# Kernel optimization log

Hardware: AMD Instinct MI355X
Metric: run time of the kernel (lower is better)

Reference implementation:

```python
import jax, jax.numpy as jnp
import numpy as np

B, N, E = 8, 2000, 32000
LAT, STY, NF = 128, 64, 10
HEADS, HID = 4, 128
OUT = 3 + NF  # 13
EPS = 1e-5
SLOPE = 0.2


def _lin(k, fi, fo):
    return jax.random.normal(k, (fi, fo), dtype=jnp.float32) / np.sqrt(fi)


def setup_inputs() -> dict:
    key = jax.random.key(0)
    ks = jax.random.split(key, 32)
    inp = {
        'z': jax.random.normal(ks[0], (B, LAT), dtype=jnp.float32),
        'template_x': jax.random.normal(ks[1], (N, NF), dtype=jnp.float32),
        'template_edge_index': jax.random.randint(ks[2], (2, E), 0, N, dtype=jnp.int32),
        # style MLP
        'mlp_w1': _lin(ks[3], LAT, 256), 'mlp_b1': jnp.zeros((256,), jnp.float32),
        'mlp_w2': _lin(ks[4], 256, 512), 'mlp_b2': jnp.zeros((512,), jnp.float32),
        'mlp_w3': _lin(ks[5], 512, STY), 'mlp_b3': jnp.zeros((STY,), jnp.float32),
        # GAT1: in = NF + STY = 74 -> heads*HID = 512, concat
        'gat1_w': _lin(ks[6], NF + STY, HEADS * HID),
        'gat1_as': jax.random.normal(ks[7], (HEADS, HID), jnp.float32) * 0.1,
        'gat1_ad': jax.random.normal(ks[8], (HEADS, HID), jnp.float32) * 0.1,
        'gat1_b': jnp.zeros((HEADS * HID,), jnp.float32),
        'ln1_g': jnp.ones((HEADS * HID,), jnp.float32), 'ln1_b': jnp.zeros((HEADS * HID,), jnp.float32),
        # GAT2: 512 -> 512, concat
        'gat2_w': _lin(ks[9], HEADS * HID, HEADS * HID),
        'gat2_as': jax.random.normal(ks[10], (HEADS, HID), jnp.float32) * 0.1,
        'gat2_ad': jax.random.normal(ks[11], (HEADS, HID), jnp.float32) * 0.1,
        'gat2_b': jnp.zeros((HEADS * HID,), jnp.float32),
        'ln2_g': jnp.ones((HEADS * HID,), jnp.float32), 'ln2_b': jnp.zeros((HEADS * HID,), jnp.float32),
        # GAT3: 512 -> 13, 1 head, no concat
        'gat3_w': _lin(ks[12], HEADS * HID, OUT),
        'gat3_as': jax.random.normal(ks[13], (1, OUT), jnp.float32) * 0.1,
        'gat3_ad': jax.random.normal(ks[14], (1, OUT), jnp.float32) * 0.1,
        'gat3_b': jnp.zeros((OUT,), jnp.float32),
    }
    return inp


def gat_conv(x, src, dst, n_nodes, W, a_src, a_dst, bias, heads, out_ch, concat):
    # x: [NT, F_in]; per-head linear transform
    h = (x @ W).reshape(-1, heads, out_ch)              # [NT, H, C]
    als = jnp.sum(h * a_src[None], axis=-1)             # [NT, H]
    ald = jnp.sum(h * a_dst[None], axis=-1)             # [NT, H]
    logits = jax.nn.leaky_relu(als[src] + ald[dst], SLOPE)   # [E, H]
    # segment softmax over destination nodes (self-loops guarantee nonempty segments)
    mx = jax.ops.segment_max(logits, dst, num_segments=n_nodes)
    alpha = jnp.exp(logits - mx[dst])
    den = jax.ops.segment_sum(alpha, dst, num_segments=n_nodes)
    alpha = alpha / den[dst]                             # [E, H]
    msgs = h[src] * alpha[:, :, None]                    # [E, H, C]
    out = jax.ops.segment_sum(msgs, dst, num_segments=n_nodes)  # [NT, H, C]
    if concat:
        return out.reshape(n_nodes, heads * out_ch) + bias
    return out.mean(axis=1) + bias


def layer_norm(x, g, b):
    mu = jnp.mean(x, axis=-1, keepdims=True)
    var = jnp.mean((x - mu) ** 2, axis=-1, keepdims=True)
    return (x - mu) * jax.lax.rsqrt(var + EPS) * g + b


def reference(z, template_x, template_edge_index,
              mlp_w1, mlp_b1, mlp_w2, mlp_b2, mlp_w3, mlp_b3,
              gat1_w, gat1_as, gat1_ad, gat1_b, ln1_g, ln1_b,
              gat2_w, gat2_as, gat2_ad, gat2_b, ln2_g, ln2_b,
              gat3_w, gat3_as, gat3_ad, gat3_b):
    bsz = z.shape[0]
    n = template_x.shape[0]
    nt = bsz * n
    # batch the template graph: replicate nodes, offset edge indices per graph
    x = jnp.tile(template_x, (bsz, 1))                                  # [NT, NF]
    off = (jnp.arange(bsz, dtype=template_edge_index.dtype) * n)
    ei = (template_edge_index[:, None, :] + off[None, :, None]).reshape(2, -1)  # [2, B*E]
    loops = jnp.arange(nt, dtype=ei.dtype)
    src = jnp.concatenate([ei[0], loops])
    dst = jnp.concatenate([ei[1], loops])
    # style MLP
    s = jax.nn.leaky_relu(z @ mlp_w1 + mlp_b1, SLOPE)
    s = jax.nn.leaky_relu(s @ mlp_w2 + mlp_b2, SLOPE)
    s = s @ mlp_w3 + mlp_b3                                             # [B, STY]
    s_exp = jnp.repeat(s, n, axis=0)                                    # [NT, STY]
    H0 = jnp.concatenate([x, s_exp], axis=1)
    H1 = jax.nn.leaky_relu(gat_conv(H0, src, dst, nt, gat1_w, gat1_as, gat1_ad, gat1_b, HEADS, HID, True), SLOPE)
    H1n = layer_norm(H1, ln1_g, ln1_b)
    H2 = jax.nn.leaky_relu(gat_conv(H1n, src, dst, nt, gat2_w, gat2_as, gat2_ad, gat2_b, HEADS, HID, True), SLOPE)
    H2 = H2 + H1n
    H2n = layer_norm(H2, ln2_g, ln2_b)
    H_out = gat_conv(H2n, src, dst, nt, gat3_w, gat3_as, gat3_ad, gat3_b, 1, OUT, False)  # [NT, 13]
    delta_p = H_out[:, :3]
    delta_f = H_out[:, 3:]
    p_gen = x[:, :3] + delta_p
    X_gen = jnp.concatenate([p_gen, x[:, 3:] + delta_f[:, 3:]], axis=1)  # X[:, :3] overwritten by p_gen
    EF = p_gen[ei[1]] - p_gen[ei[0]]                                     # edge displacement vectors [B*E, 3]
    return X_gen, p_gen, EF
```

## Files before the change

kernel.cpp:

```cpp
#include <hip/hip_runtime.h>

constexpr int Bz = 8, Nn = 2000, Ee = 32000, NTOT = 16000;
constexpr int XG_OFF = 0, PG_OFF = 160000, EF_OFF = 208000;
#define SLOPE 0.2f
#define EPSL 1e-5f

typedef __attribute__((ext_vector_type(8))) short short8v;
typedef __attribute__((ext_vector_type(4))) float float4v;

__device__ __forceinline__ float lrelu(float x) { return x > 0.f ? x : SLOPE * x; }

__device__ __forceinline__ unsigned short f2bf(float x) {
  union { float f; unsigned int u; } v; v.f = x;
  unsigned int r = v.u + 0x7fffu + ((v.u >> 16) & 1u);
  return (unsigned short)(r >> 16);
}
__device__ __forceinline__ float bf2f(unsigned int u) {
  return __uint_as_float(u << 16);
}

__device__ __forceinline__ float wave_max(float v) {
  for (int o = 32; o; o >>= 1) v = fmaxf(v, __shfl_xor(v, o));
  return v;
}
__device__ __forceinline__ float wave_sum(float v) {
  for (int o = 32; o; o >>= 1) v += __shfl_xor(v, o);
  return v;
}

__global__ void hist_k(const int* __restrict__ tei, int* __restrict__ counts) {
  int j = blockIdx.x * 256 + threadIdx.x;
  if (j < Ee) atomicAdd(&counts[tei[Ee + j]], 1);
}

__global__ void scan_k(const int* __restrict__ counts, int* __restrict__ offs) {
  __shared__ int part[256];
  int t = threadIdx.x;
  int loc[8];
  int s = 0;
  for (int i = 0; i < 8; i++) {
    int idx = t * 8 + i;
    int c = (idx < Nn) ? counts[idx] : 0;
    loc[i] = s; s += c;
  }
  part[t] = s;
  __syncthreads();
  for (int o = 1; o < 256; o <<= 1) {
    int v = (t >= o) ? part[t - o] : 0;
    __syncthreads();
    part[t] += v;
    __syncthreads();
  }
  int excl = (t == 0) ? 0 : part[t - 1];
  for (int i = 0; i < 8; i++) {
    int idx = t * 8 + i;
    if (idx < Nn) offs[idx] = excl + loc[i];
  }
  if (t == 255) offs[Nn] = part[255];
}

__global__ void place_k(const int* __restrict__ tei, const int* __restrict__ offs,
                        int* __restrict__ cursor, int* __restrict__ colb) {
  int j = blockIdx.x * 256 + threadIdx.x;
  if (j < Ee) {
    int d = tei[Ee + j];
    int slot = offs[d] + atomicAdd(&cursor[d], 1);
    colb[slot] = tei[j];
  }
}

template <int K, int ACT>
__global__ __launch_bounds__(256) void lin_k(const float* __restrict__ x, const float* __restrict__ w,
                                             const float* __restrict__ bias, float* __restrict__ y,
                                             int O) {
  int gw = blockIdx.x * 4 + (threadIdx.x >> 6);
  int lane = threadIdx.x & 63;
  int bb = gw / O, o = gw - bb * O;
  float acc = 0.f;
#pragma unroll
  for (int k = lane; k < K; k += 64) acc += x[bb * K + k] * w[k * O + o];
  acc = wave_sum(acc);
  if (lane == 0) {
    if (bias) acc += bias[o];
    y[gw] = ACT ? lrelu(acc) : acc;
  }
}

__global__ __launch_bounds__(256) void w2bf_k(const float* __restrict__ W, unsigned short* __restrict__ Bt) {
  __shared__ float tile[32][33];
  int tx = threadIdx.x & 31, ty = threadIdx.x >> 5;
  int x0 = blockIdx.x * 32;
  int y0 = blockIdx.y * 32;
  for (int r = ty; r < 32; r += 8) tile[r][tx] = W[(y0 + r) * 512 + x0 + tx];
  __syncthreads();
  for (int r = ty; r < 32; r += 8) Bt[(x0 + r) * 512 + (y0 + tx)] = f2bf(tile[tx][r]);
}

__global__ void w3t_k(const float* __restrict__ W, unsigned short* __restrict__ W3t) {
  for (int idx = threadIdx.x; idx < 8192; idx += 256) {
    int col = idx >> 9, k = idx & 511;
    float v = (col < 13) ? W[k * 13 + col] : 0.f;
    W3t[idx] = f2bf(v);
  }
}

__global__ __launch_bounds__(256) void h1_k(const float* __restrict__ tx, const float* __restrict__ g1w,
                                            const float* __restrict__ pb,
                                            const float* __restrict__ a_s, const float* __restrict__ a_d,
                                            unsigned short* __restrict__ h1, float* __restrict__ als,
                                            float* __restrict__ ald) {
  int blk = blockIdx.x;
  int b = blk & 7, nl = blk >> 3;
  int n = b * Nn + nl;
  int head = threadIdx.x >> 6, lane = threadIdx.x & 63;
  int c = head * 128 + 2 * lane;
  float t0 = 0.f, t1 = 0.f;
#pragma unroll
  for (int k = 0; k < 10; k++) {
    float xv = tx[nl * 10 + k];
    float2 wv = *(const float2*)&g1w[k * 512 + c];
    t0 += xv * wv.x; t1 += xv * wv.y;
  }
  float2 pv = *(const float2*)&pb[b * 512 + c];
  float hx = t0 + pv.x, hy = t1 + pv.y;
  ushort2 st; st.x = f2bf(hx); st.y = f2bf(hy);
  *(ushort2*)&h1[(size_t)n * 512 + c] = st;
  float2 av = *(const float2*)&a_s[c];
  float2 dv = *(const float2*)&a_d[c];
  float pa = wave_sum(hx * av.x + hy * av.y);
  float pd = wave_sum(hx * dv.x + hy * dv.y);
  if (lane == 0) { als[n * 4 + head] = pa; ald[n * 4 + head] = pd; }
}

template <int RESID>
__global__ __launch_bounds__(256) void agg_k(const unsigned short* __restrict__ h,
                                             const float* __restrict__ als, const float* __restrict__ ald,
                                             const float* __restrict__ bias,
                                             const float* __restrict__ g, const float* __restrict__ beta,
                                             const unsigned short* __restrict__ resid,
                                             unsigned short* __restrict__ out,
                                             const int* __restrict__ offs, const int* __restrict__ colb) {
  int blk = blockIdx.x;
  int b = blk & 7, nl = blk >> 3;
  int n = b * Nn + nl;
  int w = threadIdx.x >> 6, lane = threadIdx.x & 63;
  int li = lane & 15, eg = lane >> 4;
  int rs = offs[nl];
  int nit = offs[nl + 1] - rs + 1;
  float aldn = ald[n * 4 + w];

  __shared__ float alpha_s[4][64];
  __shared__ int sgn[64];
  __shared__ float fin[512];

  float accv[8] = {0.f, 0.f, 0.f, 0.f, 0.f, 0.f, 0.f, 0.f};
  float inv;
  const unsigned short* hbase = h + (size_t)w * 128 + li * 8;

  if (nit <= 64) {
    int sg = n;
    float logit = -3e38f;
    if (lane < nit) {
      sg = (lane < nit - 1) ? colb[rs + lane] + b * Nn : n;
      logit = lrelu(als[sg * 4 + w] + aldn);
      if (w == 0) sgn[lane] = sg;
    }
    float m = wave_max(logit);
    float raw = (lane < nit) ? __expf(logit - m) : 0.f;
    inv = 1.f / wave_sum(raw);
    if (lane < nit) alpha_s[w][lane] = raw;
    __syncthreads();
    for (int e = eg; e < nit; e += 4) {
      float a = alpha_s[w][e];
      uint4 hv = *(const uint4*)(hbase + (size_t)sgn[e] * 512);
      accv[0] += a * bf2f(hv.x & 0xffffu); accv[1] += a * bf2f(hv.x >> 16);
      accv[2] += a * bf2f(hv.y & 0xffffu); accv[3] += a * bf2f(hv.y >> 16);
      accv[4] += a * bf2f(hv.z & 0xffffu); accv[5] += a * bf2f(hv.z >> 16);
      accv[6] += a * bf2f(hv.w & 0xffffu); accv[7] += a * bf2f(hv.w >> 16);
    }
    __syncthreads();
  } else {
    float m = -3e38f;
    for (int i = lane; i < nit; i += 64) {
      int sg = (i < nit - 1) ? colb[rs + i] + b * Nn : n;
      m = fmaxf(m, lrelu(als[sg * 4 + w] + aldn));
    }
    m = wave_max(m);
    float den = 0.f;
    for (int base = 0; base < nit; base += 64) {
      int cnt = min(64, nit - base);
      float raw = 0.f;
      if (lane < cnt) {
        int i = base + lane;
        int sg = (i < nit - 1) ? colb[rs + i] + b * Nn : n;
        raw = __expf(lrelu(als[sg * 4 + w] + aldn) - m);
        if (w == 0) sgn[lane] = sg;
        alpha_s[w][lane] = raw;
      }
      den += raw;
      __syncthreads();
      for (int e = eg; e < cnt; e += 4) {
        float a = alpha_s[w][e];
        uint4 hv = *(const uint4*)(hbase + (size_t)sgn[e] * 512);
        accv[0] += a * bf2f(hv.x & 0xffffu); accv[1] += a * bf2f(hv.x >> 16);
        accv[2] += a * bf2f(hv.y & 0xffffu); accv[3] += a * bf2f(hv.y >> 16);
        accv[4] += a * bf2f(hv.z & 0xffffu); accv[5] += a * bf2f(hv.z >> 16);
        accv[6] += a * bf2f(hv.w & 0xffffu); accv[7] += a * bf2f(hv.w >> 16);
      }
      __syncthreads();
    }
    inv = 1.f / wave_sum(den);
  }

#pragma unroll
  for (int j = 0; j < 8; j++) {
    accv[j] += __shfl_xor(accv[j], 16);
    accv[j] += __shfl_xor(accv[j], 32);
  }
  if (eg == 0) {
#pragma unroll
    for (int j = 0; j < 8; j++) fin[w * 128 + li * 8 + j] = accv[j] * inv;
  }
  __syncthreads();

  int c = 2 * threadIdx.x;
  float v0 = lrelu(fin[c] + bias[c]);
  float v1 = lrelu(fin[c + 1] + bias[c + 1]);
  if (RESID) {
    unsigned int rv = *(const unsigned int*)&resid[(size_t)n * 512 + c];
    v0 += bf2f(rv & 0xffffu); v1 += bf2f(rv >> 16);
  }
  __shared__ float red[8];
  __shared__ float bc[2];
  float p1 = wave_sum(v0 + v1);
  float p2 = wave_sum(v0 * v0 + v1 * v1);
  if (lane == 0) { red[w] = p1; red[4 + w] = p2; }
  __syncthreads();
  if (threadIdx.x == 0) {
    float s1 = red[0] + red[1] + red[2] + red[3];
    float s2 = red[4] + red[5] + red[6] + red[7];
    float mu = s1 * (1.f / 512.f);
    float var = s2 * (1.f / 512.f) - mu * mu;
    bc[0] = mu;
    bc[1] = rsqrtf(var + EPSL);
  }
  __syncthreads();
  float mu = bc[0], rstd = bc[1];
  float o0 = (v0 - mu) * rstd * g[c] + beta[c];
  float o1 = (v1 - mu) * rstd * g[c + 1] + beta[c + 1];
  ushort2 st; st.x = f2bf(o0); st.y = f2bf(o1);
  *(ushort2*)&out[(size_t)n * 512 + c] = st;
}

__global__ __launch_bounds__(256) void gemm2_k(const unsigned short* __restrict__ A,
                                               const unsigned short* __restrict__ Bt,
                                               unsigned short* __restrict__ C,
                                               const float* __restrict__ As, const float* __restrict__ Ad,
                                               float* __restrict__ als2, float* __restrict__ ald2) {
  __shared__ char smem[32768];
  char* sAc = smem;
  char* sBc = smem + 16384;
  int t = threadIdx.x;
  int lane = t & 63, w = t >> 6;
  int wr = w >> 1, wc = w & 1;
  int m0 = blockIdx.y * 128, n0 = blockIdx.x * 128;
  int head = blockIdx.x;

  float4v acc[4][4];
#pragma unroll
  for (int i = 0; i < 4; i++)
#pragma unroll
    for (int j = 0; j < 4; j++) acc[i][j] = (float4v){0.f, 0.f, 0.f, 0.f};

  int srow[4], sklin[4], ssw[4];
#pragma unroll
  for (int i = 0; i < 4; i++) {
    int slot = i * 256 + t;
    srow[i] = slot >> 3;
    sklin[i] = (slot & 7) * 16;
    ssw[i] = srow[i] * 128 + (sklin[i] ^ ((srow[i] & 7) << 4));
  }

  uint4 va[4], vb[4];
#pragma unroll
  for (int i = 0; i < 4; i++) {
    va[i] = *(const uint4*)((const char*)A + (size_t)(m0 + srow[i]) * 1024 + sklin[i]);
    vb[i] = *(const uint4*)((const char*)Bt + (size_t)(n0 + srow[i]) * 1024 + sklin[i]);
  }

  int r_a = wr * 64 + (lane & 15);
  int r_b = wc * 64 + (lane & 15);
  int kbb = (lane >> 4) * 16;
  int sw_a = (r_a & 7) << 4;
  int sw_b = (r_b & 7) << 4;

  for (int k0 = 0; k0 < 512; k0 += 64) {
    if (k0) __syncthreads();
#pragma unroll
    for (int i = 0; i < 4; i++) {
      *(uint4*)(sAc + ssw[i]) = va[i];
      *(uint4*)(sBc + ssw[i]) = vb[i];
    }
    __syncthreads();
    if (k0 + 64 < 512) {
#pragma unroll
      for (int i = 0; i < 4; i++) {
        va[i] = *(const uint4*)((const char*)A + (size_t)(m0 + srow[i]) * 1024 + (k0 + 64) * 2 + sklin[i]);
        vb[i] = *(const uint4*)((const char*)Bt + (size_t)(n0 + srow[i]) * 1024 + (k0 + 64) * 2 + sklin[i]);
      }
    }
#pragma unroll
    for (int ksub = 0; ksub < 2; ksub++) {
      short8v af[4], bg[4];
#pragma unroll
      for (int m = 0; m < 4; m++)
        af[m] = *(const short8v*)(sAc + (r_a + m * 16) * 128 + ((ksub * 64 + kbb) ^ sw_a));
#pragma unroll
      for (int nn = 0; nn < 4; nn++)
        bg[nn] = *(const short8v*)(sBc + (r_b + nn * 16) * 128 + ((ksub * 64 + kbb) ^ sw_b));
#pragma unroll
      for (int m = 0; m < 4; m++)
#pragma unroll
        for (int nn = 0; nn < 4; nn++)
          acc[m][nn] = __builtin_amdgcn_mfma_f32_16x16x32_bf16(af[m], bg[nn], acc[m][nn], 0, 0, 0);
    }
  }

  int orow = m0 + wr * 64 + (lane >> 4) * 4;
  int ocol = n0 + wc * 64 + (lane & 15);
#pragma unroll
  for (int m = 0; m < 4; m++)
#pragma unroll
    for (int nn = 0; nn < 4; nn++)
#pragma unroll
      for (int r = 0; r < 4; r++)
        C[(size_t)(orow + m * 16 + r) * 512 + ocol + nn * 16] = f2bf(acc[m][nn][r]);

  __syncthreads();
  float* sRed = (float*)smem;
  int cidx0 = wc * 64 + (lane & 15);
  float asv[4], adv[4];
#pragma unroll
  for (int nn = 0; nn < 4; nn++) {
    asv[nn] = As[head * 128 + cidx0 + nn * 16];
    adv[nn] = Ad[head * 128 + cidx0 + nn * 16];
  }
#pragma unroll
  for (int m = 0; m < 4; m++) {
#pragma unroll
    for (int r = 0; r < 4; r++) {
      float pa = 0.f, pd = 0.f;
#pragma unroll
      for (int nn = 0; nn < 4; nn++) { pa += acc[m][nn][r] * asv[nn]; pd += acc[m][nn][r] * adv[nn]; }
      for (int o = 1; o < 16; o <<= 1) { pa += __shfl_xor(pa, o); pd += __shfl_xor(pd, o); }
      if ((lane & 15) == 0) {
        int rblk = wr * 64 + (lane >> 4) * 4 + m * 16 + r;
        sRed[rblk * 2 + wc] = pa;
        sRed[256 + rblk * 2 + wc] = pd;
      }
    }
  }
  __syncthreads();
  if (t < 128) {
    als2[(m0 + t) * 4 + head] = sRed[t * 2] + sRed[t * 2 + 1];
  } else {
    int r2 = t - 128;
    ald2[(m0 + r2) * 4 + head] = sRed[256 + r2 * 2] + sRed[256 + r2 * 2 + 1];
  }
}

__global__ __launch_bounds__(256) void gemm3_k(const unsigned short* __restrict__ H,
                                               const unsigned short* __restrict__ W3t,
                                               const float* __restrict__ as3, const float* __restrict__ ad3,
                                               float* __restrict__ h3, float* __restrict__ als3,
                                               float* __restrict__ ald3) {
  int w = threadIdx.x >> 6, l = threadIdx.x & 63;
  int m0 = blockIdx.x * 64 + w * 16;
  int r16 = l & 15, g4 = l >> 4;
  float4v acc = (float4v){0.f, 0.f, 0.f, 0.f};
  const unsigned short* ha = H + (size_t)(m0 + r16) * 512 + g4 * 8;
  const unsigned short* wb = W3t + (size_t)r16 * 512 + g4 * 8;
#pragma unroll
  for (int kk = 0; kk < 16; kk++) {
    short8v a = *(const short8v*)(ha + kk * 32);
    short8v bfr = *(const short8v*)(wb + kk * 32);
    acc = __builtin_amdgcn_mfma_f32_16x16x32_bf16(a, bfr, acc, 0, 0, 0);
  }
  int col = r16;
  float asv = (col < 13) ? as3[col] : 0.f;
  float adv = (col < 13) ? ad3[col] : 0.f;
#pragma unroll
  for (int r = 0; r < 4; r++) {
    float v = acc[r];
    int row = m0 + g4 * 4 + r;
    if (col < 13) h3[row * 13 + col] = v;
    float sa = v * asv, sd = v * adv;
    for (int o = 1; o < 16; o <<= 1) { sa += __shfl_xor(sa, o); sd += __shfl_xor(sd, o); }
    if (col == 0) { als3[row] = sa; ald3[row] = sd; }
  }
}

__global__ __launch_bounds__(64) void agg3_k(const float* __restrict__ h3, const float* __restrict__ als3,
                                             const float* __restrict__ ald3, const float* __restrict__ b3,
                                             const float* __restrict__ tx, const int* __restrict__ offs,
                                             const int* __restrict__ colb, float* __restrict__ dout) {
  int blk = blockIdx.x, lane = threadIdx.x;
  int b = blk & 7, nl = blk >> 3;
  int n = b * Nn + nl;
  int rs = offs[nl], deg = offs[nl + 1] - rs;
  float aldn = ald3[n];
  float sl = lrelu(als3[n] + aldn);
  float a = 0.f, inv;
  if (deg <= 64) {
    int sgl = 0; float logit = -1e30f;
    if (lane < deg) { sgl = colb[rs + lane] + b * Nn; logit = lrelu(als3[sgl] + aldn); }
    float m = wave_max(fmaxf(logit, sl));
    float raw = (lane < deg) ? __expf(logit - m) : 0.f;
    float es = __expf(sl - m);
    inv = 1.f / (wave_sum(raw) + es);
    if (lane < 13) a = es * h3[n * 13 + lane];
    for (int e = 0; e < deg; e++) {
      float w = __shfl(raw, e);
      int sg = __shfl(sgl, e);
      if (lane < 13) a += w * h3[sg * 13 + lane];
    }
  } else {
    float m = sl;
    for (int e = lane; e < deg; e += 64) {
      int sg = colb[rs + e] + b * Nn;
      m = fmaxf(m, lrelu(als3[sg] + aldn));
    }
    m = wave_max(m);
    float es = __expf(sl - m);
    float den = (lane == 0) ? es : 0.f;
    if (lane < 13) a = es * h3[n * 13 + lane];
    for (int base = 0; base < deg; base += 64) {
      int cnt = min(64, deg - base);
      int sgl = 0; float raw = 0.f;
      if (lane < cnt) {
        sgl = colb[rs + base + lane] + b * Nn;
        raw = __expf(lrelu(als3[sgl] + aldn) - m);
      }
      den += raw;
      for (int e = 0; e < cnt; e++) {
        float w = __shfl(raw, e);
        int sg = __shfl(sgl, e);
        if (lane < 13) a += w * h3[sg * 13 + lane];
      }
    }
    inv = 1.f / wave_sum(den);
  }
  a *= inv;
  float hv = a + ((lane < 13) ? b3[lane] : 0.f);
  float txv = (lane < 10) ? tx[nl * 10 + lane] : 0.f;
  float pv = txv + hv;
  if (lane < 3) dout[PG_OFF + n * 3 + lane] = pv;
  float up = __shfl(hv, lane + 3);
  float xg = (lane < 3) ? pv : (txv + up);
  if (lane < 10) dout[XG_OFF + n * 10 + lane] = xg;
}

__global__ void ef_k(const int* __restrict__ tei, float* __restrict__ dout) {
  int e = blockIdx.x * 256 + threadIdx.x;
  int b = e / Ee, j = e - b * Ee;
  int sg = tei[j] + b * Nn;
  int dg = tei[Ee + j] + b * Nn;
  const float* pg = dout + PG_OFF;
  dout[EF_OFF + e * 3 + 0] = pg[dg * 3 + 0] - pg[sg * 3 + 0];
  dout[EF_OFF + e * 3 + 1] = pg[dg * 3 + 1] - pg[sg * 3 + 1];
  dout[EF_OFF + e * 3 + 2] = pg[dg * 3 + 2] - pg[sg * 3 + 2];
}

extern "C" void kernel_launch(void* const* d_in, const int* in_sizes, int n_in,
                              void* d_out, int out_size, void* d_ws, size_t ws_size,
                              hipStream_t stream) {
  const float* z = (const float*)d_in[0];
  const float* tx = (const float*)d_in[1];
  const int* tei = (const int*)d_in[2];
  const float* w1 = (const float*)d_in[3];
  const float* b1 = (const float*)d_in[4];
  const float* w2 = (const float*)d_in[5];
  const float* b2 = (const float*)d_in[6];
  const float* w3 = (const float*)d_in[7];
  const float* b3 = (const float*)d_in[8];
  const float* g1w = (const float*)d_in[9];
  const float* g1as = (const float*)d_in[10];
  const float* g1ad = (const float*)d_in[11];
  const float* g1b = (const float*)d_in[12];
  const float* ln1g = (const float*)d_in[13];
  const float* ln1b = (const float*)d_in[14];
  const float* g2w = (const float*)d_in[15];
  const float* g2as = (const float*)d_in[16];
  const float* g2ad = (const float*)d_in[17];
  const float* g2b = (const float*)d_in[18];
  const float* ln2g = (const float*)d_in[19];
  const float* ln2b = (const float*)d_in[20];
  const float* g3w = (const float*)d_in[21];
  const float* g3as = (const float*)d_in[22];
  const float* g3ad = (const float*)d_in[23];
  const float* g3b = (const float*)d_in[24];
  float* out = (float*)d_out;

  float* F = (float*)d_ws;
  float* pb_ = F + 0;
  float* l1_ = F + 8192;
  float* l2_ = F + 16384;
  float* s_ = F + 24576;
  float* als1 = F + 100000;
  float* ald1 = F + 164000;
  float* als2 = F + 228000;
  float* ald2 = F + 292000;
  float* als3 = F + 356000;
  float* ald3 = F + 372000;
  float* h3_ = F + 388000;
  unsigned short* U = (unsigned short*)(F + 600000);
  unsigned short* hA = U;
  unsigned short* hB = U + 8192000;
  unsigned short* Bt = U + 16384000;
  unsigned short* W3t = U + 16646144;
  int* I = (int*)(F + 10000000);
  int* counts = I;
  int* cursor = I + 2000;
  int* offs = I + 4000;
  int* colb = I + 6001;

  hipMemsetAsync(counts, 0, 4000 * sizeof(int), stream);
  hist_k<<<125, 256, 0, stream>>>(tei, counts);
  scan_k<<<1, 256, 0, stream>>>(counts, offs);
  place_k<<<125, 256, 0, stream>>>(tei, offs, cursor, colb);

  w2bf_k<<<dim3(16, 16), 256, 0, stream>>>(g2w, Bt);
  w3t_k<<<1, 256, 0, stream>>>(g3w, W3t);

  lin_k<128, 1><<<512, 256, 0, stream>>>(z, w1, b1, l1_, 256);
  lin_k<256, 1><<<1024, 256, 0, stream>>>(l1_, w2, b2, l2_, 512);
  lin_k<512, 0><<<128, 256, 0, stream>>>(l2_, w3, b3, s_, 64);
  lin_k<64, 0><<<1024, 256, 0, stream>>>(s_, g1w + 10 * 512, nullptr, pb_, 512);

  h1_k<<<NTOT, 256, 0, stream>>>(tx, g1w, pb_, g1as, g1ad, hA, als1, ald1);
  agg_k<0><<<NTOT, 256, 0, stream>>>(hA, als1, ald1, g1b, ln1g, ln1b, nullptr, hB, offs, colb);

  gemm2_k<<<dim3(4, 125), 256, 0, stream>>>(hB, Bt, hA, g2as, g2ad, als2, ald2);
  agg_k<1><<<NTOT, 256, 0, stream>>>(hA, als2, ald2, g2b, ln2g, ln2b, hB, hB, offs, colb);

  gemm3_k<<<250, 256, 0, stream>>>(hB, W3t, g3as, g3ad, h3_, als3, ald3);
  agg3_k<<<NTOT, 64, 0, stream>>>(h3_, als3, ald3, g3b, tx, offs, colb, out);
  ef_k<<<1000, 256, 0, stream>>>(tei, out);
}
```

Measured before the change: 236.9 us.

## Switch intermediate storage to fp16 and aggregate with packed half2 FMAs

Converts all stored intermediates and GEMM operands from bf16 to fp16, using the fp16 MFMA instruction. The aggregation kernel now accumulates neighbour features with packed __hfma2 in half precision. Attention weights and source indices are broadcast via wave shuffles instead of being staged through shared memory, which removes two block barriers per chunk. This cuts ALU work in the gather loop, at the risk of fp16 overflow or precision loss in the accumulations, since the unnormalised exp weights are summed in half.

```diff
diff --git a/kernel.cpp b/kernel.cpp
--- a/kernel.cpp
+++ b/kernel.cpp
@@ -1,22 +1,19 @@
 #include <hip/hip_runtime.h>
+#include <hip/hip_fp16.h>
 
 constexpr int Bz = 8, Nn = 2000, Ee = 32000, NTOT = 16000;
 constexpr int XG_OFF = 0, PG_OFF = 160000, EF_OFF = 208000;
 #define SLOPE 0.2f
 #define EPSL 1e-5f
 
-typedef __attribute__((ext_vector_type(8))) short short8v;
+typedef __attribute__((ext_vector_type(8))) _Float16 f16x8;
 typedef __attribute__((ext_vector_type(4))) float float4v;
 
 __device__ __forceinline__ float lrelu(float x) { return x > 0.f ? x : SLOPE * x; }
 
-__device__ __forceinline__ unsigned short f2bf(float x) {
-  union { float f; unsigned int u; } v; v.f = x;
-  unsigned int r = v.u + 0x7fffu + ((v.u >> 16) & 1u);
-  return (unsigned short)(r >> 16);
-}
-__device__ __forceinline__ float bf2f(unsigned int u) {
-  return __uint_as_float(u << 16);
+__device__ __forceinline__ unsigned short f2h(float x) {
+  _Float16 hh = (_Float16)x;
+  return *(unsigned short*)&hh;
 }
 
 __device__ __forceinline__ float wave_max(float v) {
@@ -93,14 +90,14 @@
   int y0 = blockIdx.y * 32;
   for (int r = ty; r < 32; r += 8) tile[r][tx] = W[(y0 + r) * 512 + x0 + tx];
   __syncthreads();
-  for (int r = ty; r < 32; r += 8) Bt[(x0 + r) * 512 + (y0 + tx)] = f2bf(tile[tx][r]);
+  for (int r = ty; r < 32; r += 8) Bt[(x0 + r) * 512 + (y0 + tx)] = f2h(tile[tx][r]);
 }
 
 __global__ void w3t_k(const float* __restrict__ W, unsigned short* __restrict__ W3t) {
   for (int idx = threadIdx.x; idx < 8192; idx += 256) {
     int col = idx >> 9, k = idx & 511;
     float v = (col < 13) ? W[k * 13 + col] : 0.f;
-    W3t[idx] = f2bf(v);
+    W3t[idx] = f2h(v);
   }
 }
 
@@ -123,7 +120,7 @@
   }
   float2 pv = *(const float2*)&pb[b * 512 + c];
   float hx = t0 + pv.x, hy = t1 + pv.y;
-  ushort2 st; st.x = f2bf(hx); st.y = f2bf(hy);
+  ushort2 st; st.x = f2h(hx); st.y = f2h(hy);
   *(ushort2*)&h1[(size_t)n * 512 + c] = st;
   float2 av = *(const float2*)&a_s[c];
   float2 dv = *(const float2*)&a_d[c];
@@ -149,13 +146,15 @@
   int nit = offs[nl + 1] - rs + 1;
   float aldn = ald[n * 4 + w];
 
-  __shared__ float alpha_s[4][64];
-  __shared__ int sgn[64];
   __shared__ float fin[512];
-
-  float accv[8] = {0.f, 0.f, 0.f, 0.f, 0.f, 0.f, 0.f, 0.f};
+  __shared__ float red[8];
+  __shared__ float bcs[2];
+
+  __half2 acc2[4];
+#pragma unroll
+  for (int j = 0; j < 4; j++) acc2[j] = __float2half2_rn(0.f);
   float inv;
-  const unsigned short* hbase = h + (size_t)w * 128 + li * 8;
+  const unsigned short* hbase = h + (size_t)(w * 128 + li * 8);
 
   if (nit <= 64) {
     int sg = n;
@@ -163,22 +162,22 @@
     if (lane < nit) {
       sg = (lane < nit - 1) ? colb[rs + lane] + b * Nn : n;
       logit = lrelu(als[sg * 4 + w] + aldn);
-      if (w == 0) sgn[lane] = sg;
     }
     float m = wave_max(logit);
     float raw = (lane < nit) ? __expf(logit - m) : 0.f;
     inv = 1.f / wave_sum(raw);
-    if (lane < nit) alpha_s[w][lane] = raw;
-    __syncthreads();
+    __half2 a2r = __float2half2_rn(raw);
+    int au = *(int*)&a2r;
     for (int e = eg; e < nit; e += 4) {
-      float a = alpha_s[w][e];
-      uint4 hv = *(const uint4*)(hbase + (size_t)sgn[e] * 512);
-      accv[0] += a * bf2f(hv.x & 0xffffu); accv[1] += a * bf2f(hv.x >> 16);
-      accv[2] += a * bf2f(hv.y & 0xffffu); accv[3] += a * bf2f(hv.y >> 16);
-      accv[4] += a * bf2f(hv.z & 0xffffu); accv[5] += a * bf2f(hv.z >> 16);
-      accv[6] += a * bf2f(hv.w & 0xffffu); accv[7] += a * bf2f(hv.w >> 16);
-    }
-    __syncthreads();
+      int aeu = __shfl(au, e);
+      int sge = __shfl(sg, e);
+      __half2 a2 = *(__half2*)&aeu;
+      uint4 hv = *(const uint4*)(hbase + (size_t)sge * 512);
+      acc2[0] = __hfma2(a2, *(__half2*)&hv.x, acc2[0]);
+      acc2[1] = __hfma2(a2, *(__half2*)&hv.y, acc2[1]);
+      acc2[2] = __hfma2(a2, *(__half2*)&hv.z, acc2[2]);
+      acc2[3] = __hfma2(a2, *(__half2*)&hv.w, acc2[3]);
+    }
   } else {
     float m = -3e38f;
     for (int i = lane; i < nit; i += 64) {
@@ -189,37 +188,44 @@
     float den = 0.f;
     for (int base = 0; base < nit; base += 64) {
       int cnt = min(64, nit - base);
+      int sg = n;
       float raw = 0.f;
       if (lane < cnt) {
         int i = base + lane;
-        int sg = (i < nit - 1) ? colb[rs + i] + b * Nn : n;
+        sg = (i < nit - 1) ? colb[rs + i] + b * Nn : n;
         raw = __expf(lrelu(als[sg * 4 + w] + aldn) - m);
-        if (w == 0) sgn[lane] = sg;
-        alpha_s[w][lane] = raw;
       }
       den += raw;
-      __syncthreads();
+      __half2 a2r = __float2half2_rn(raw);
+      int au = *(int*)&a2r;
       for (int e = eg; e < cnt; e += 4) {
-        float a = alpha_s[w][e];
-        uint4 hv = *(const uint4*)(hbase + (size_t)sgn[e] * 512);
-        accv[0] += a * bf2f(hv.x & 0xffffu); accv[1] += a * bf2f(hv.x >> 16);
-        accv[2] += a * bf2f(hv.y & 0xffffu); accv[3] += a * bf2f(hv.y >> 16);
-        accv[4] += a * bf2f(hv.z & 0xffffu); accv[5] += a * bf2f(hv.z >> 16);
-        accv[6] += a * bf2f(hv.w & 0xffffu); accv[7] += a * bf2f(hv.w >> 16);
+        int aeu = __shfl(au, e);
+        int sge = __shfl(sg, e);
+        __half2 a2 = *(__half2*)&aeu;
+        uint4 hv = *(const uint4*)(hbase + (size_t)sge * 512);
+        acc2[0] = __hfma2(a2, *(__half2*)&hv.x, acc2[0]);
+        acc2[1] = __hfma2(a2, *(__half2*)&hv.y, acc2[1]);
+        acc2[2] = __hfma2(a2, *(__half2*)&hv.z, acc2[2]);
+        acc2[3] = __hfma2(a2, *(__half2*)&hv.w, acc2[3]);
       }
-      __syncthreads();
     }
     inv = 1.f / wave_sum(den);
   }
 
+  float fv[8];
+#pragma unroll
+  for (int j = 0; j < 4; j++) {
+    float2 f2 = __half22float2(acc2[j]);
+    fv[2 * j] = f2.x; fv[2 * j + 1] = f2.y;
+  }
 #pragma unroll
   for (int j = 0; j < 8; j++) {
-    accv[j] += __shfl_xor(accv[j], 16);
-    accv[j] += __shfl_xor(accv[j], 32);
+    fv[j] += __shfl_xor(fv[j], 16);
+    fv[j] += __shfl_xor(fv[j], 32);
   }
   if (eg == 0) {
 #pragma unroll
-    for (int j = 0; j < 8; j++) fin[w * 128 + li * 8 + j] = accv[j] * inv;
+    for (int j = 0; j < 8; j++) fin[w * 128 + li * 8 + j] = fv[j] * inv;
   }
   __syncthreads();
 
@@ -228,10 +234,10 @@
   float v1 = lrelu(fin[c + 1] + bias[c + 1]);
   if (RESID) {
     unsigned int rv = *(const unsigned int*)&resid[(size_t)n * 512 + c];
-    v0 += bf2f(rv & 0xffffu); v1 += bf2f(rv >> 16);
-  }
-  __shared__ float red[8];
-  __shared__ float bc[2];
+    __half2 rh = *(__half2*)&rv;
+    float2 rf = __half22float2(rh);
+    v0 += rf.x; v1 += rf.y;
+  }
   float p1 = wave_sum(v0 + v1);
   float p2 = wave_sum(v0 * v0 + v1 * v1);
   if (lane == 0) { red[w] = p1; red[4 + w] = p2; }
@@ -241,14 +247,14 @@
     float s2 = red[4] + red[5] + red[6] + red[7];
     float mu = s1 * (1.f / 512.f);
     float var = s2 * (1.f / 512.f) - mu * mu;
-    bc[0] = mu;
-    bc[1] = rsqrtf(var + EPSL);
-  }
-  __syncthreads();
-  float mu = bc[0], rstd = bc[1];
+    bcs[0] = mu;
+    bcs[1] = rsqrtf(var + EPSL);
+  }
+  __syncthreads();
+  float mu = bcs[0], rstd = bcs[1];
   float o0 = (v0 - mu) * rstd * g[c] + beta[c];
   float o1 = (v1 - mu) * rstd * g[c + 1] + beta[c + 1];
-  ushort2 st; st.x = f2bf(o0); st.y = f2bf(o1);
+  ushort2 st; st.x = f2h(o0); st.y = f2h(o1);
   *(ushort2*)&out[(size_t)n * 512 + c] = st;
 }
 
@@ -311,18 +317,18 @@
     }
 #pragma unroll
     for (int ksub = 0; ksub < 2; ksub++) {
-      short8v af[4], bg[4];
+      f16x8 af[4], bg[4];
 #pragma unroll
       for (int m = 0; m < 4; m++)
-        af[m] = *(const short8v*)(sAc + (r_a + m * 16) * 128 + ((ksub * 64 + kbb) ^ sw_a));
+        af[m] = *(const f16x8*)(sAc + (r_a + m * 16) * 128 + ((ksub * 64 + kbb) ^ sw_a));
 #pragma unroll
       for (int nn = 0; nn < 4; nn++)
-        bg[nn] = *(const short8v*)(sBc + (r_b + nn * 16) * 128 + ((ksub * 64 + kbb) ^ sw_b));
+        bg[nn] = *(const f16x8*)(sBc + (r_b + nn * 16) * 128 + ((ksub * 64 + kbb) ^ sw_b));
 #pragma unroll
       for (int m = 0; m < 4; m++)
 #pragma unroll
         for (int nn = 0; nn < 4; nn++)
-          acc[m][nn] = __builtin_amdgcn_mfma_f32_16x16x32_bf16(af[m], bg[nn], acc[m][nn], 0, 0, 0);
+          acc[m][nn] = __builtin_amdgcn_mfma_f32_16x16x32_f16(af[m], bg[nn], acc[m][nn], 0, 0, 0);
     }
   }
 
@@ -334,7 +340,7 @@
     for (int nn = 0; nn < 4; nn++)
 #pragma unroll
       for (int r = 0; r < 4; r++)
-        C[(size_t)(orow + m * 16 + r) * 512 + ocol + nn * 16] = f2bf(acc[m][nn][r]);
+        C[(size_t)(orow + m * 16 + r) * 512 + ocol + nn * 16] = f2h(acc[m][nn][r]);
 
   __syncthreads();
   float* sRed = (float*)smem;
@@ -382,9 +388,9 @@
   const unsigned short* wb = W3t + (size_t)r16 * 512 + g4 * 8;
 #pragma unroll
   for (int kk = 0; kk < 16; kk++) {
-    short8v a = *(const short8v*)(ha + kk * 32);
-    short8v bfr = *(const short8v*)(wb + kk * 32);
-    acc = __builtin_amdgcn_mfma_f32_16x16x32_bf16(a, bfr, acc, 0, 0, 0);
+    f16x8 a = *(const f16x8*)(ha + kk * 32);
+    f16x8 bfr = *(const f16x8*)(wb + kk * 32);
+    acc = __builtin_amdgcn_mfma_f32_16x16x32_f16(a, bfr, acc, 0, 0, 0);
   }
   int col = r16;
   float asv = (col < 13) ? as3[col] : 0.f;
```

Result: no change. 235.2 us (-0.7%).
